# Performance work log

Hardware: AMD Instinct MI355X
Metric: run time of the kernel (lower is better)

Reference implementation:

```python
import jax, jax.numpy as jnp
import numpy as np

N_RAYS = 65536   # 256x256 image
T_SAMPLES = 128  # StratifiedRayStepSampler default
HID = 16         # tiny radiance-field MLP hidden width


def setup_inputs() -> dict:
    key = jax.random.key(0)
    ks = jax.random.split(key, 8)
    o = jax.random.normal(ks[0], (N_RAYS, 3), jnp.float32)
    d = jax.random.normal(ks[1], (N_RAYS, 3), jnp.float32)
    tnear = jnp.zeros((N_RAYS, 1), jnp.float32)
    # tfar in [1,5): guarantees tfar > tnear for every ray
    tfar = 1.0 + 4.0 * jax.random.uniform(ks[2], (N_RAYS, 1), jnp.float32)
    noise = jax.random.uniform(ks[3], (T_SAMPLES, N_RAYS, 1), jnp.float32)
    W1 = jax.random.normal(ks[4], (3, HID), jnp.float32) * 0.5
    b1 = jnp.zeros((HID,), jnp.float32)
    w_sigma = jax.random.normal(ks[5], (HID, 1), jnp.float32) * 0.5
    W_rgb = jax.random.normal(ks[6], (HID, 3), jnp.float32) * 0.5
    return {"o": o, "d": d, "tnear": tnear, "tfar": tfar, "noise": noise,
            "W1": W1, "b1": b1, "w_sigma": w_sigma, "W_rgb": W_rgb}


def reference(o, d, tnear, tfar, noise, W1, b1, w_sigma, W_rgb):
    T = noise.shape[0]
    dnorm = jnp.linalg.norm(d, axis=-1, keepdims=True)            # (N,1)
    # stratified sampling: ts[i] = tnear + (tfar-tnear)*(i+u_i)/T  -> (T,N,1)
    bins = (jnp.arange(T, dtype=o.dtype)[:, None, None] + noise) / T
    ts = tnear[None] + (tfar - tnear)[None] * bins                # (T,N,1)
    # evaluate rays and query radiance field
    xyz = o[None] + ts * d[None]                                  # (T,N,3)
    h = jax.nn.relu(xyz @ W1 + b1)                                # (T,N,HID)
    sigma = jax.nn.softplus(h @ w_sigma)                          # (T,N,1) density
    rgb = jax.nn.sigmoid(h @ W_rgb)                               # (T,N,3) color
    # volumetric integration along sample axis
    delta = jnp.concatenate([ts[1:] - ts[:-1], tfar[None] - ts[-1:]], axis=0)
    sd = sigma * delta * dnorm[None]                              # (T,N,1)
    # exclusive cumsum -> log-transmittance (stable cumprod)
    log_trans = jnp.concatenate(
        [jnp.zeros_like(sd[:1]), -jnp.cumsum(sd[:-1], axis=0)], axis=0)
    weights = jnp.exp(log_trans) * (1.0 - jnp.exp(-sd))           # (T,N,1)
    color = jnp.sum(weights * rgb, axis=0)                        # (N,3)
    depth = jnp.sum(weights * ts, axis=0)                         # (N,1)
    alpha = jnp.sum(weights, axis=0)                              # (N,1)
    return jnp.concatenate([color, depth, alpha], axis=-1)        # (N,5)
```

## Files before the change

### kernel.cpp

```cpp
#include <hip/hip_runtime.h>
#include <math.h>

#define N_RAYS 65536
#define T_SAMPLES 128
#define HID 16

#define RAYS_PER_BLOCK 64
#define CHUNKS 4
#define CHUNK_LEN (T_SAMPLES / CHUNKS)

#define L2E 1.4426950408889634f

__global__ __launch_bounds__(256, 4) void radiance_kernel(
    const float* __restrict__ o,
    const float* __restrict__ d,
    const float* __restrict__ tnear,
    const float* __restrict__ tfar,
    const float* __restrict__ noise,
    const float* __restrict__ W1,
    const float* __restrict__ b1,
    const float* __restrict__ w_sigma,
    const float* __restrict__ W_rgb,
    float* __restrict__ out)
{
    const int lane  = threadIdx.x & 63;
    const int chunk = threadIdx.x >> 6;
    const int ray   = blockIdx.x * RAYS_PER_BLOCK + lane;

    const float ox = o[ray*3+0], oy = o[ray*3+1], oz = o[ray*3+2];
    const float dx = d[ray*3+0], dy = d[ray*3+1], dz = d[ray*3+2];
    const float tn = tnear[ray];
    const float tf = tfar[ray];
    const float dnorm = sqrtf(dx*dx + dy*dy + dz*dz);
    const float sc = (tf - tn) * (1.0f / (float)T_SAMPLES);

    float A[HID], B[HID];
#pragma unroll
    for (int j = 0; j < HID; ++j) {
        const float w0 = W1[0*HID + j], w1 = W1[1*HID + j], w2 = W1[2*HID + j];
        A[j] = fmaf(ox, w0, fmaf(oy, w1, fmaf(oz, w2, b1[j])));
        B[j] = fmaf(dx, w0, fmaf(dy, w1, dz * w2));
    }
    float WS[HID], WR[HID], WG[HID], WB[HID];
#pragma unroll
    for (int j = 0; j < HID; ++j) {
        WS[j] = w_sigma[j];
        WR[j] = W_rgb[j*3+0];
        WG[j] = W_rgb[j*3+1];
        WB[j] = W_rgb[j*3+2];
    }

    const int t0 = chunk * CHUNK_LEN;
    const float nz0 = noise[(size_t)t0 * N_RAYS + ray];
    float fi = (float)t0;
    float ts = fmaf(sc, fi + nz0, tn);

    float lt = 1.0f;
    float cr = 0.f, cg = 0.f, cb = 0.f, cd = 0.f, ca = 0.f;

    for (int i = 0; i < CHUNK_LEN; ++i) {
        const int t = t0 + i;
        const bool has_next = (t + 1 < T_SAMPLES);
        float nz_next = 0.0f;
        if (has_next) nz_next = noise[(size_t)(t+1) * N_RAYS + ray];

        float sp = 0.f, rr = 0.f, gg = 0.f, bb = 0.f;
#pragma unroll
        for (int j = 0; j < HID; ++j) {
            const float h = fmaxf(fmaf(ts, B[j], A[j]), 0.0f);
            sp = fmaf(h, WS[j], sp);
            rr = fmaf(h, WR[j], rr);
            gg = fmaf(h, WG[j], gg);
            bb = fmaf(h, WB[j], bb);
        }

        const float ts_next = has_next ? fmaf(sc, fi + 1.0f + nz_next, tn) : tf;

        const float e  = __builtin_amdgcn_exp2f(-fabsf(sp) * L2E);
        const float l2 = fmaf(fmaxf(sp, 0.0f), L2E, __builtin_amdgcn_logf(1.0f + e));
        const float dd = (ts_next - ts) * dnorm;
        const float et = __builtin_amdgcn_exp2f(-dd * l2);

        const float r = __builtin_amdgcn_rcpf(1.0f + __builtin_amdgcn_exp2f(-rr * L2E));
        const float g = __builtin_amdgcn_rcpf(1.0f + __builtin_amdgcn_exp2f(-gg * L2E));
        const float b = __builtin_amdgcn_rcpf(1.0f + __builtin_amdgcn_exp2f(-bb * L2E));

        const float w = lt * (1.0f - et);
        cr = fmaf(w, r, cr);
        cg = fmaf(w, g, cg);
        cb = fmaf(w, b, cb);
        cd = fmaf(w, ts, cd);
        ca += w;
        lt *= et;
        ts = ts_next;
        fi += 1.0f;
    }

    __shared__ float s_lt[CHUNKS][RAYS_PER_BLOCK];
    __shared__ float s_acc[CHUNKS][5][RAYS_PER_BLOCK];
    s_lt[chunk][lane] = lt;
    s_acc[chunk][0][lane] = cr;
    s_acc[chunk][1][lane] = cg;
    s_acc[chunk][2][lane] = cb;
    s_acc[chunk][3][lane] = cd;
    s_acc[chunk][4][lane] = ca;
    __syncthreads();

    if (chunk == 0) {
        float scale = 1.0f;
        float a0 = 0.f, a1 = 0.f, a2 = 0.f, a3 = 0.f, a4 = 0.f;
#pragma unroll
        for (int c = 0; c < CHUNKS; ++c) {
            a0 = fmaf(scale, s_acc[c][0][lane], a0);
            a1 = fmaf(scale, s_acc[c][1][lane], a1);
            a2 = fmaf(scale, s_acc[c][2][lane], a2);
            a3 = fmaf(scale, s_acc[c][3][lane], a3);
            a4 = fmaf(scale, s_acc[c][4][lane], a4);
            scale *= s_lt[c][lane];
        }
        out[ray*5+0] = a0;
        out[ray*5+1] = a1;
        out[ray*5+2] = a2;
        out[ray*5+3] = a3;
        out[ray*5+4] = a4;
    }
}

extern "C" void kernel_launch(void* const* d_in, const int* in_sizes, int n_in,
                              void* d_out, int out_size, void* d_ws, size_t ws_size,
                              hipStream_t stream) {
    const float* o       = (const float*)d_in[0];
    const float* d       = (const float*)d_in[1];
    const float* tnear   = (const float*)d_in[2];
    const float* tfar    = (const float*)d_in[3];
    const float* noise   = (const float*)d_in[4];
    const float* W1      = (const float*)d_in[5];
    const float* b1      = (const float*)d_in[6];
    const float* w_sigma = (const float*)d_in[7];
    const float* W_rgb   = (const float*)d_in[8];
    float* out = (float*)d_out;

    dim3 block(64 * CHUNKS);
    dim3 grid(N_RAYS / RAYS_PER_BLOCK);
    hipLaunchKernelGGL(radiance_kernel, grid, block, 0, stream,
                       o, d, tnear, tfar, noise, W1, b1, w_sigma, W_rgb, out);
}
```

Before: 115.4 us.

## Prefetch chunk noise into registers and split rays into eight sample chunks

Each block now handles 32 rays with 8 sample chunks per ray, so each thread integrates 16 samples instead of 32. Each thread loads all of its noise values, plus the next chunk's first value, into registers before the loop and fully unrolls the loop. This removes the dependent global load on every iteration and exposes more parallelism across threads. In exchange, per-thread setup is repeated for twice as many threads, each wave now reads two half-width noise rows, register pressure rises, and the final sample's end point is computed arithmetically from `tf` rather than using it directly.

```diff
diff --git a/kernel.cpp b/kernel.cpp
--- a/kernel.cpp
+++ b/kernel.cpp
@@ -5,8 +5,8 @@
 #define T_SAMPLES 128
 #define HID 16
 
-#define RAYS_PER_BLOCK 64
-#define CHUNKS 4
+#define RAYS_PER_BLOCK 32
+#define CHUNKS 8
 #define CHUNK_LEN (T_SAMPLES / CHUNKS)
 
 #define L2E 1.4426950408889634f
@@ -23,9 +23,22 @@
     const float* __restrict__ W_rgb,
     float* __restrict__ out)
 {
-    const int lane  = threadIdx.x & 63;
-    const int chunk = threadIdx.x >> 6;
-    const int ray   = blockIdx.x * RAYS_PER_BLOCK + lane;
+    __shared__ float s_lt[CHUNKS * RAYS_PER_BLOCK];
+    __shared__ float s_acc[CHUNKS * 5 * RAYS_PER_BLOCK];
+
+    const int ridx  = threadIdx.x & 31;
+    const int chunk = threadIdx.x >> 5;
+    const int ray   = blockIdx.x * RAYS_PER_BLOCK + ridx;
+    const int t0    = chunk * CHUNK_LEN;
+
+    float nzv[CHUNK_LEN + 1];
+#pragma unroll
+    for (int k = 0; k <= CHUNK_LEN; ++k) {
+        const int tt = t0 + k;
+        const int tc = tt < T_SAMPLES ? tt : T_SAMPLES - 1;
+        nzv[k] = noise[(size_t)tc * N_RAYS + ray];
+    }
+    if (t0 + CHUNK_LEN >= T_SAMPLES) nzv[CHUNK_LEN] = 0.0f;
 
     const float ox = o[ray*3+0], oy = o[ray*3+1], oz = o[ray*3+2];
     const float dx = d[ray*3+0], dy = d[ray*3+1], dz = d[ray*3+2];
@@ -50,19 +63,15 @@
         WB[j] = W_rgb[j*3+2];
     }
 
-    const int t0 = chunk * CHUNK_LEN;
-    const float nz0 = noise[(size_t)t0 * N_RAYS + ray];
-    float fi = (float)t0;
-    float ts = fmaf(sc, fi + nz0, tn);
+    const float t0f = (float)t0;
+    float ts = fmaf(sc, t0f + nzv[0], tn);
 
     float lt = 1.0f;
     float cr = 0.f, cg = 0.f, cb = 0.f, cd = 0.f, ca = 0.f;
 
-    for (int i = 0; i < CHUNK_LEN; ++i) {
-        const int t = t0 + i;
-        const bool has_next = (t + 1 < T_SAMPLES);
-        float nz_next = 0.0f;
-        if (has_next) nz_next = noise[(size_t)(t+1) * N_RAYS + ray];
+#pragma unroll
+    for (int k = 0; k < CHUNK_LEN; ++k) {
+        const float ts_next = fmaf(sc, t0f + (float)(k + 1) + nzv[k + 1], tn);
 
         float sp = 0.f, rr = 0.f, gg = 0.f, bb = 0.f;
 #pragma unroll
@@ -74,18 +83,15 @@
             bb = fmaf(h, WB[j], bb);
         }
 
-        const float ts_next = has_next ? fmaf(sc, fi + 1.0f + nz_next, tn) : tf;
-
         const float e  = __builtin_amdgcn_exp2f(-fabsf(sp) * L2E);
         const float l2 = fmaf(fmaxf(sp, 0.0f), L2E, __builtin_amdgcn_logf(1.0f + e));
-        const float dd = (ts_next - ts) * dnorm;
-        const float et = __builtin_amdgcn_exp2f(-dd * l2);
+        const float et = __builtin_amdgcn_exp2f((ts - ts_next) * dnorm * l2);
 
         const float r = __builtin_amdgcn_rcpf(1.0f + __builtin_amdgcn_exp2f(-rr * L2E));
         const float g = __builtin_amdgcn_rcpf(1.0f + __builtin_amdgcn_exp2f(-gg * L2E));
         const float b = __builtin_amdgcn_rcpf(1.0f + __builtin_amdgcn_exp2f(-bb * L2E));
 
-        const float w = lt * (1.0f - et);
+        const float w = fmaf(-lt, et, lt);
         cr = fmaf(w, r, cr);
         cg = fmaf(w, g, cg);
         cb = fmaf(w, b, cb);
@@ -93,30 +99,27 @@
         ca += w;
         lt *= et;
         ts = ts_next;
-        fi += 1.0f;
     }
 
-    __shared__ float s_lt[CHUNKS][RAYS_PER_BLOCK];
-    __shared__ float s_acc[CHUNKS][5][RAYS_PER_BLOCK];
-    s_lt[chunk][lane] = lt;
-    s_acc[chunk][0][lane] = cr;
-    s_acc[chunk][1][lane] = cg;
-    s_acc[chunk][2][lane] = cb;
-    s_acc[chunk][3][lane] = cd;
-    s_acc[chunk][4][lane] = ca;
+    s_lt[chunk * RAYS_PER_BLOCK + ridx] = lt;
+    s_acc[(chunk * 5 + 0) * RAYS_PER_BLOCK + ridx] = cr;
+    s_acc[(chunk * 5 + 1) * RAYS_PER_BLOCK + ridx] = cg;
+    s_acc[(chunk * 5 + 2) * RAYS_PER_BLOCK + ridx] = cb;
+    s_acc[(chunk * 5 + 3) * RAYS_PER_BLOCK + ridx] = cd;
+    s_acc[(chunk * 5 + 4) * RAYS_PER_BLOCK + ridx] = ca;
     __syncthreads();
 
-    if (chunk == 0) {
+    if (threadIdx.x < RAYS_PER_BLOCK) {
         float scale = 1.0f;
         float a0 = 0.f, a1 = 0.f, a2 = 0.f, a3 = 0.f, a4 = 0.f;
 #pragma unroll
         for (int c = 0; c < CHUNKS; ++c) {
-            a0 = fmaf(scale, s_acc[c][0][lane], a0);
-            a1 = fmaf(scale, s_acc[c][1][lane], a1);
-            a2 = fmaf(scale, s_acc[c][2][lane], a2);
-            a3 = fmaf(scale, s_acc[c][3][lane], a3);
-            a4 = fmaf(scale, s_acc[c][4][lane], a4);
-            scale *= s_lt[c][lane];
+            a0 = fmaf(scale, s_acc[(c * 5 + 0) * RAYS_PER_BLOCK + ridx], a0);
+            a1 = fmaf(scale, s_acc[(c * 5 + 1) * RAYS_PER_BLOCK + ridx], a1);
+            a2 = fmaf(scale, s_acc[(c * 5 + 2) * RAYS_PER_BLOCK + ridx], a2);
+            a3 = fmaf(scale, s_acc[(c * 5 + 3) * RAYS_PER_BLOCK + ridx], a3);
+            a4 = fmaf(scale, s_acc[(c * 5 + 4) * RAYS_PER_BLOCK + ridx], a4);
+            scale *= s_lt[c * RAYS_PER_BLOCK + ridx];
         }
         out[ray*5+0] = a0;
         out[ray*5+1] = a1;
@@ -140,7 +143,7 @@
     const float* W_rgb   = (const float*)d_in[8];
     float* out = (float*)d_out;
 
-    dim3 block(64 * CHUNKS);
+    dim3 block(RAYS_PER_BLOCK * CHUNKS);
     dim3 grid(N_RAYS / RAYS_PER_BLOCK);
     hipLaunchKernelGGL(radiance_kernel, grid, block, 0, stream,
                        o, d, tnear, tfar, noise, W1, b1, w_sigma, W_rgb, out);
```

New measurement: 121.1 us. 1.05x slower.
